# Kernel optimization log

Measured on AMD Instinct MI355X. Metric: run time of the kernel, lower is better.

## Reference

```python
import jax, jax.numpy as jnp
import numpy as np

H = 768
NH = 12
HD = H // NH
NDIM = 5
LN_EPS = 1e-5


def setup_inputs() -> dict:
    key = jax.random.key(0)
    ks = jax.random.split(key, 12)
    B, S = 4, 2048
    xavier = lambda k: jax.random.uniform(k, (H, H), jnp.float32, -1.0, 1.0) * np.sqrt(6.0 / (H + H))
    return {
        "hidden_states": jax.random.normal(ks[0], (B, S, H), jnp.float32),
        "Wq": xavier(ks[1]), "bq": jnp.zeros((H,), jnp.float32),
        "Wk": xavier(ks[2]), "bk": jnp.zeros((H,), jnp.float32),
        "Wv": xavier(ks[3]), "bv": jnp.zeros((H,), jnp.float32),
        "Wo": xavier(ks[4]), "bo": jnp.zeros((H,), jnp.float32),
        # per-dimension, per-head scalar biases (torch init: zeros; use small randn so grads are non-trivial)
        "dim_biases": 0.02 * jax.random.normal(ks[5], (NDIM, NH), jnp.float32),
        "ln_gamma": jnp.ones((H,), jnp.float32),
        "ln_beta": jnp.zeros((H,), jnp.float32),
        "attention_mask": jax.random.randint(ks[6], (4, 2048), 0, 2, jnp.int32),
        "dimension_idx": 2,
    }


def reference(hidden_states, Wq, bq, Wk, bk, Wv, bv, Wo, bo, dim_biases,
              ln_gamma, ln_beta, attention_mask, dimension_idx):
    B, S, _ = hidden_states.shape
    residual = hidden_states
    # torch nn.Linear: x @ W.T + b
    q = (hidden_states @ Wq.T + bq).reshape(B, S, NH, HD).transpose(0, 2, 1, 3)  # [B,NH,S,HD]
    k = (hidden_states @ Wk.T + bk).reshape(B, S, NH, HD).transpose(0, 2, 1, 3)
    v = (hidden_states @ Wv.T + bv).reshape(B, S, NH, HD).transpose(0, 2, 1, 3)

    scores = jnp.einsum("bhqd,bhkd->bhqk", q, k) / np.sqrt(HD)  # [B,NH,S,S]
    if dimension_idx is not None and dimension_idx < NDIM:
        scores = scores + dim_biases[dimension_idx][None, :, None, None]
    # mask over key positions, broadcast over heads and queries
    scores = jnp.where(attention_mask[:, None, None, :] == 0, -jnp.inf, scores)
    attn = jax.nn.softmax(scores, axis=-1)

    ctx = jnp.einsum("bhqk,bhkd->bhqd", attn, v)  # [B,NH,S,HD]
    ctx = ctx.transpose(0, 2, 1, 3).reshape(B, S, H)
    out = ctx @ Wo.T + bo

    y = out + residual
    mu = jnp.mean(y, axis=-1, keepdims=True)
    var = jnp.var(y, axis=-1, keepdims=True)
    y = (y - mu) / jnp.sqrt(var + LN_EPS) * ln_gamma + ln_beta
    return y
```

## Files before the change

kernel.cpp:

```cpp
#include <hip/hip_runtime.h>
#include <hip/hip_bf16.h>

#define HH    768
#define NHEAD 12
#define HDIM  64
#define BB    4
#define SS    2048
#define MM    (BB*SS)
#define NDIMS 5
#define WEL   (HH*HH)
#define LOG2E 1.44269504088896f
#define QSCALE 0.180336881f

typedef unsigned short u16;
typedef __attribute__((ext_vector_type(8))) short short8;
typedef __attribute__((ext_vector_type(4))) float floatx4;

__device__ __forceinline__ float bf2f(u16 u) {
    return __uint_as_float(((unsigned int)u) << 16);
}
__device__ __forceinline__ u16 f2bf(float f) {
    unsigned int x = __float_as_uint(f);
    unsigned int r = (x + 0x7fffu + ((x >> 16) & 1u)) >> 16;
    return (u16)r;
}
__device__ __forceinline__ unsigned int pack_bf16x2(float a, float b) {
    float2 f2 = make_float2(a, b);
    __hip_bfloat162 h2 = __float22bfloat162_rn(f2);
    return *reinterpret_cast<unsigned int*>(&h2);
}

__global__ __launch_bounds__(256) void f32_to_bf16(
    const float* __restrict__ in, u16* __restrict__ out, int n8)
{
    int i = blockIdx.x * 256 + threadIdx.x;
    if (i >= n8) return;
    float4 a = ((const float4*)in)[i*2];
    float4 b = ((const float4*)in)[i*2 + 1];
    ushort4 lo, hi;
    lo.x = f2bf(a.x); lo.y = f2bf(a.y); lo.z = f2bf(a.z); lo.w = f2bf(a.w);
    hi.x = f2bf(b.x); hi.y = f2bf(b.y); hi.z = f2bf(b.z); hi.w = f2bf(b.w);
    ((ushort4*)out)[i*2]     = lo;
    ((ushort4*)out)[i*2 + 1] = hi;
}

__global__ __launch_bounds__(256) void w_cvt4(
    const float* __restrict__ W0, const float* __restrict__ W1,
    const float* __restrict__ W2, const float* __restrict__ W3,
    u16* __restrict__ out)
{
    const float* src = (blockIdx.y == 0) ? W0 : (blockIdx.y == 1) ? W1
                     : (blockIdx.y == 2) ? W2 : W3;
    u16* dst = out + (size_t)blockIdx.y * WEL;
    int i = blockIdx.x * 256 + threadIdx.x;
    float4 a = ((const float4*)src)[i*2];
    float4 b = ((const float4*)src)[i*2 + 1];
    ushort4 lo, hi;
    lo.x = f2bf(a.x); lo.y = f2bf(a.y); lo.z = f2bf(a.z); lo.w = f2bf(a.w);
    hi.x = f2bf(b.x); hi.y = f2bf(b.y); hi.z = f2bf(b.z); hi.w = f2bf(b.w);
    ((ushort4*)dst)[i*2]     = lo;
    ((ushort4*)dst)[i*2 + 1] = hi;
}

__device__ __forceinline__ void gemm_body_bb(
    const u16* __restrict__ Xb, const u16* __restrict__ Wb,
    const float* __restrict__ bias, u16* __restrict__ out,
    int i0, int j0)
{
    __shared__ u16 Xs[128][40];
    __shared__ u16 Wt[64][40];
    const int t = threadIdx.x;
    const int w = t >> 6, lane = t & 63;
    const int c = lane & 15, qd = lane >> 4;
    const int xrow = t >> 1, xoff = (t & 1) * 16;
    const int wn = t >> 2, woff = (t & 3) * 8;

    floatx4 acc[2][4];
    #pragma unroll
    for (int mt = 0; mt < 2; ++mt)
        #pragma unroll
        for (int nt = 0; nt < 4; ++nt) acc[mt][nt] = (floatx4){0.f,0.f,0.f,0.f};

    for (int k0 = 0; k0 < HH; k0 += 32) {
        uint4 xa  = *(const uint4*)(Xb + (size_t)(i0 + xrow)*HH + k0 + xoff);
        uint4 xb2 = *(const uint4*)(Xb + (size_t)(i0 + xrow)*HH + k0 + xoff + 8);
        uint4 wa  = *(const uint4*)(Wb + (size_t)(j0 + wn)*HH + k0 + woff);
        __syncthreads();
        *(uint4*)&Xs[xrow][xoff]     = xa;
        *(uint4*)&Xs[xrow][xoff + 8] = xb2;
        *(uint4*)&Wt[wn][woff]       = wa;
        __syncthreads();

        short8 a0 = *(const short8*)&Xs[w*32 + c][qd*8];
        short8 a1 = *(const short8*)&Xs[w*32 + 16 + c][qd*8];
        #pragma unroll
        for (int nt = 0; nt < 4; ++nt) {
            short8 bfr = *(const short8*)&Wt[nt*16 + c][qd*8];
            acc[0][nt] = __builtin_amdgcn_mfma_f32_16x16x32_bf16(a0, bfr, acc[0][nt], 0, 0, 0);
            acc[1][nt] = __builtin_amdgcn_mfma_f32_16x16x32_bf16(a1, bfr, acc[1][nt], 0, 0, 0);
        }
    }

    float bv[4];
    #pragma unroll
    for (int nt = 0; nt < 4; ++nt) bv[nt] = bias[j0 + nt*16 + c];
    #pragma unroll
    for (int mt = 0; mt < 2; ++mt)
        #pragma unroll
        for (int nt = 0; nt < 4; ++nt)
            #pragma unroll
            for (int r = 0; r < 4; ++r)
                out[(size_t)(i0 + w*32 + mt*16 + qd*4 + r)*HH + j0 + nt*16 + c] =
                    f2bf(acc[mt][nt][r] + bv[nt]);
}

__global__ __launch_bounds__(256) void gemm_mfma_qkv(
    const u16* __restrict__ Xb, const u16* __restrict__ Wb3,
    const float* __restrict__ bq, const float* __restrict__ bk, const float* __restrict__ bv,
    u16* __restrict__ oq, u16* __restrict__ ok, u16* __restrict__ ov)
{
    const int z = blockIdx.z;
    const u16* W = Wb3 + (size_t)z * WEL;
    const float* bias = (z == 0) ? bq : (z == 1) ? bk : bv;
    u16* out = (z == 0) ? oq : (z == 1) ? ok : ov;
    gemm_body_bb(Xb, W, bias, out, blockIdx.y * 128, blockIdx.x * 64);
}

__global__ __launch_bounds__(256) void gemm_mfma_nt_bb(
    const u16* __restrict__ Xb, const u16* __restrict__ Wb,
    const float* __restrict__ bias, u16* __restrict__ out)
{
    gemm_body_bb(Xb, Wb, bias, out, blockIdx.y * 128, blockIdx.x * 64);
}

__global__ __launch_bounds__(256) void gemm_mfma_nt(
    const u16* __restrict__ Xb, const float* __restrict__ W,
    const float* __restrict__ bias, u16* __restrict__ out)
{
    __shared__ u16 Xs[128][40];
    __shared__ u16 Wt[64][40];
    const int t = threadIdx.x;
    const int w = t >> 6, lane = t & 63;
    const int c = lane & 15, qd = lane >> 4;
    const int i0 = blockIdx.y * 128, j0 = blockIdx.x * 64;
    const int xrow = t >> 1, xoff = (t & 1) * 16;
    const int wn = t >> 2, woff = (t & 3) * 8;

    floatx4 acc[2][4];
    #pragma unroll
    for (int mt = 0; mt < 2; ++mt)
        #pragma unroll
        for (int nt = 0; nt < 4; ++nt) acc[mt][nt] = (floatx4){0.f,0.f,0.f,0.f};

    for (int k0 = 0; k0 < HH; k0 += 32) {
        uint4 xa  = *(const uint4*)(Xb + (size_t)(i0 + xrow)*HH + k0 + xoff);
        uint4 xb2 = *(const uint4*)(Xb + (size_t)(i0 + xrow)*HH + k0 + xoff + 8);
        float4 wa = *(const float4*)(W + (size_t)(j0 + wn)*HH + k0 + woff);
        float4 wb = *(const float4*)(W + (size_t)(j0 + wn)*HH + k0 + woff + 4);
        __syncthreads();
        *(uint4*)&Xs[xrow][xoff]     = xa;
        *(uint4*)&Xs[xrow][xoff + 8] = xb2;
        ushort4 w0, w1;
        w0.x = f2bf(wa.x); w0.y = f2bf(wa.y); w0.z = f2bf(wa.z); w0.w = f2bf(wa.w);
        w1.x = f2bf(wb.x); w1.y = f2bf(wb.y); w1.z = f2bf(wb.z); w1.w = f2bf(wb.w);
        *(ushort4*)&Wt[wn][woff]     = w0;
        *(ushort4*)&Wt[wn][woff + 4] = w1;
        __syncthreads();

        short8 a0 = *(const short8*)&Xs[w*32 + c][qd*8];
        short8 a1 = *(const short8*)&Xs[w*32 + 16 + c][qd*8];
        #pragma unroll
        for (int nt = 0; nt < 4; ++nt) {
            short8 bfr = *(const short8*)&Wt[nt*16 + c][qd*8];
            acc[0][nt] = __builtin_amdgcn_mfma_f32_16x16x32_bf16(a0, bfr, acc[0][nt], 0, 0, 0);
            acc[1][nt] = __builtin_amdgcn_mfma_f32_16x16x32_bf16(a1, bfr, acc[1][nt], 0, 0, 0);
        }
    }

    float bv[4];
    #pragma unroll
    for (int nt = 0; nt < 4; ++nt) bv[nt] = bias[j0 + nt*16 + c];
    #pragma unroll
    for (int mt = 0; mt < 2; ++mt)
        #pragma unroll
        for (int nt = 0; nt < 4; ++nt)
            #pragma unroll
            for (int r = 0; r < 4; ++r)
                out[(size_t)(i0 + w*32 + mt*16 + qd*4 + r)*HH + j0 + nt*16 + c] =
                    f2bf(acc[mt][nt][r] + bv[nt]);
}

__global__ __launch_bounds__(256, 3) void attn_mfma(
    const u16* __restrict__ Q, const u16* __restrict__ K, const u16* __restrict__ V,
    const float* __restrict__ dim_biases, const int* __restrict__ mask,
    const int* __restrict__ dim_idx_p, u16* __restrict__ ctx)
{
    __shared__ u16 Ks[64][72];
    __shared__ u16 Vt[64][72];
    __shared__ u16 Pt[4][2][16][72];
    __shared__ float madd[64];

    const int t = threadIdx.x;
    const int w = t >> 6, lane = t & 63;
    const int c = lane & 15, qd = lane >> 4;
    const int b = blockIdx.z, h = blockIdx.y;
    const int q0 = blockIdx.x * 128;

    const int didx = *dim_idx_p;
    const float db2 = ((didx < NDIMS) ? dim_biases[didx*NHEAD + h] : 0.f) * LOG2E;

    short8 ones;
    #pragma unroll
    for (int j = 0; j < 8; ++j) ones[j] = (short)0x3F80;

    short8 qf[2][2];
    #pragma unroll
    for (int g = 0; g < 2; ++g) {
        const u16* qsrc = Q + ((size_t)(b*SS + q0 + w*32 + g*16 + c))*HH + h*HDIM;
        #pragma unroll
        for (int kc = 0; kc < 2; ++kc) {
            ushort4 u0 = *(const ushort4*)(qsrc + kc*32 + qd*8);
            ushort4 u1 = *(const ushort4*)(qsrc + kc*32 + qd*8 + 4);
            const u16 uu[8] = {u0.x,u0.y,u0.z,u0.w,u1.x,u1.y,u1.z,u1.w};
            #pragma unroll
            for (int j = 0; j < 8; ++j)
                qf[g][kc][j] = (short)f2bf(bf2f(uu[j]) * QSCALE);
        }
    }

    floatx4 o[2][4], lacc[2];
    #pragma unroll
    for (int g = 0; g < 2; ++g) {
        lacc[g] = (floatx4){0.f,0.f,0.f,0.f};
        #pragma unroll
        for (int dt = 0; dt < 4; ++dt) o[g][dt] = (floatx4){0.f,0.f,0.f,0.f};
    }

    const int skey = t >> 2, sdp = (t & 3) * 16;
    const int vkey = t & 63, vdp = (t >> 6) * 16;

    for (int kt = 0; kt < SS/64; ++kt) {
        __syncthreads();
        {
            const u16* ksrc = K + ((size_t)(b*SS + kt*64 + skey))*HH + h*HDIM + sdp;
            *(uint4*)&Ks[skey][sdp]     = *(const uint4*)ksrc;
            *(uint4*)&Ks[skey][sdp + 8] = *(const uint4*)(ksrc + 8);
            const u16* vsrc = V + ((size_t)(b*SS + kt*64 + vkey))*HH + h*HDIM + vdp;
            ushort4 v0 = *(const ushort4*)vsrc;
            ushort4 v1 = *(const ushort4*)(vsrc + 4);
            ushort4 v2 = *(const ushort4*)(vsrc + 8);
            ushort4 v3 = *(const ushort4*)(vsrc + 12);
            const u16 vv[16] = {v0.x,v0.y,v0.z,v0.w, v1.x,v1.y,v1.z,v1.w,
                                v2.x,v2.y,v2.z,v2.w, v3.x,v3.y,v3.z,v3.w};
            #pragma unroll
            for (int i = 0; i < 16; ++i) Vt[vdp + i][vkey] = vv[i];
            if (t < 64)
                madd[t] = (mask[(size_t)b*SS + kt*64 + t] != 0) ? db2 : -1e30f;
        }
        __syncthreads();

        floatx4 z[2][4];
        {
            short8 ka[4][2];
            #pragma unroll
            for (int mt = 0; mt < 4; ++mt) {
                ka[mt][0] = *(const short8*)&Ks[mt*16 + c][qd*8];
                ka[mt][1] = *(const short8*)&Ks[mt*16 + c][32 + qd*8];
            }
            #pragma unroll
            for (int g = 0; g < 2; ++g)
                #pragma unroll
                for (int mt = 0; mt < 4; ++mt) {
                    floatx4 zz = __builtin_amdgcn_mfma_f32_16x16x32_bf16(ka[mt][0], qf[g][0], (floatx4){0.f,0.f,0.f,0.f}, 0, 0, 0);
                    z[g][mt] = __builtin_amdgcn_mfma_f32_16x16x32_bf16(ka[mt][1], qf[g][1], zz, 0, 0, 0);
                }
        }

        #pragma unroll
        for (int g = 0; g < 2; ++g) {
            #pragma unroll
            for (int mt = 0; mt < 4; ++mt) {
                unsigned int pk[2];
                #pragma unroll
                for (int half = 0; half < 2; ++half) {
                    float p0 = __builtin_amdgcn_exp2f(z[g][mt][half*2]     + madd[mt*16 + qd*4 + half*2]);
                    float p1 = __builtin_amdgcn_exp2f(z[g][mt][half*2 + 1] + madd[mt*16 + qd*4 + half*2 + 1]);
                    pk[half] = pack_bf16x2(p0, p1);
                }
                *(uint2*)&Pt[w][g][c][mt*16 + qd*4] = make_uint2(pk[0], pk[1]);
            }
        }

        {
            short8 vt[2][4];
            #pragma unroll
            for (int kc = 0; kc < 2; ++kc)
                #pragma unroll
                for (int dt = 0; dt < 4; ++dt)
                    vt[kc][dt] = *(const short8*)&Vt[dt*16 + c][kc*32 + qd*8];
            #pragma unroll
            for (int g = 0; g < 2; ++g)
                #pragma unroll
                for (int kc = 0; kc < 2; ++kc) {
                    short8 ap = *(const short8*)&Pt[w][g][c][kc*32 + qd*8];
                    lacc[g] = __builtin_amdgcn_mfma_f32_16x16x32_bf16(ap, ones, lacc[g], 0, 0, 0);
                    #pragma unroll
                    for (int dt = 0; dt < 4; ++dt)
                        o[g][dt] = __builtin_amdgcn_mfma_f32_16x16x32_bf16(ap, vt[kc][dt], o[g][dt], 0, 0, 0);
                }
        }
    }

    #pragma unroll
    for (int g = 0; g < 2; ++g) {
        #pragma unroll
        for (int r = 0; r < 4; ++r) {
            float lr = lacc[g][r];
            float inv = (lr > 0.f) ? 1.f / lr : 0.f;
            u16* dst = ctx + ((size_t)(b*SS + q0 + w*32 + g*16 + qd*4 + r))*HH + h*HDIM + c;
            #pragma unroll
            for (int dt = 0; dt < 4; ++dt)
                dst[dt*16] = f2bf(o[g][dt][r] * inv);
        }
    }
}

__global__ __launch_bounds__(256) void add_ln_wave(
    const u16* __restrict__ proj, const float* __restrict__ resid,
    const float* __restrict__ gamma, const float* __restrict__ beta,
    float* __restrict__ out)
{
    const int t = threadIdx.x, w = t >> 6, lane = t & 63;
    const int row = blockIdx.x * 4 + w;
    const size_t base = (size_t)row * HH + lane * 12;
    const int gbase = lane * 12;

    float x[12];
    #pragma unroll
    for (int j = 0; j < 3; ++j) {
        ushort4 p = *(const ushort4*)(proj + base + j*4);
        float4  r = *(const float4*)(resid + base + j*4);
        x[j*4+0] = bf2f(p.x) + r.x;
        x[j*4+1] = bf2f(p.y) + r.y;
        x[j*4+2] = bf2f(p.z) + r.z;
        x[j*4+3] = bf2f(p.w) + r.w;
    }
    float s = 0.f, ss = 0.f;
    #pragma unroll
    for (int j = 0; j < 12; ++j) { s += x[j]; ss += x[j]*x[j]; }
    #pragma unroll
    for (int off = 1; off < 64; off <<= 1) {
        s  += __shfl_xor(s, off);
        ss += __shfl_xor(ss, off);
    }
    float mean = s * (1.f/768.f);
    float var  = ss * (1.f/768.f) - mean*mean;
    float rstd = rsqrtf(fmaxf(var, 0.f) + 1e-5f);
    #pragma unroll
    for (int j = 0; j < 3; ++j) {
        float4 g = *(const float4*)(gamma + gbase + j*4);
        float4 bt = *(const float4*)(beta + gbase + j*4);
        float4 y;
        y.x = (x[j*4+0]-mean)*rstd*g.x + bt.x;
        y.y = (x[j*4+1]-mean)*rstd*g.y + bt.y;
        y.z = (x[j*4+2]-mean)*rstd*g.z + bt.z;
        y.w = (x[j*4+3]-mean)*rstd*g.w + bt.w;
        *(float4*)(out + base + j*4) = y;
    }
}

extern "C" void kernel_launch(void* const* d_in, const int* in_sizes, int n_in,
                              void* d_out, int out_size, void* d_ws, size_t ws_size,
                              hipStream_t stream)
{
    (void)in_sizes; (void)n_in; (void)out_size;
    const float* x    = (const float*)d_in[0];
    const float* Wq   = (const float*)d_in[1];
    const float* bq   = (const float*)d_in[2];
    const float* Wk   = (const float*)d_in[3];
    const float* bk   = (const float*)d_in[4];
    const float* Wv   = (const float*)d_in[5];
    const float* bv   = (const float*)d_in[6];
    const float* Wo   = (const float*)d_in[7];
    const float* bo   = (const float*)d_in[8];
    const float* dimb = (const float*)d_in[9];
    const float* gam  = (const float*)d_in[10];
    const float* bet  = (const float*)d_in[11];
    const int* mask   = (const int*)d_in[12];
    const int* didx   = (const int*)d_in[13];

    const size_t N = (size_t)MM * HH;
    if (ws_size < 4 * N * sizeof(u16)) return;
    u16* ws = (u16*)d_ws;
    u16* q    = ws;
    u16* kbuf = ws + N;
    u16* vbuf = ws + 2*N;
    u16* slot3 = ws + 3*N;
    u16* xb   = slot3;
    u16* ctx  = slot3;
    u16* proj = q;

    const bool bigws = ws_size >= (4 * N + 4 * (size_t)WEL) * sizeof(u16);
    u16* wb = ws + 4 * N;

    dim3 gg(HH/64, MM/128);
    f32_to_bf16<<<(int)(N/8/256), 256, 0, stream>>>(x, xb, (int)(N/8));
    if (bigws) {
        w_cvt4<<<dim3(WEL/8/256, 4), 256, 0, stream>>>(Wq, Wk, Wv, Wo, wb);
        gemm_mfma_qkv<<<dim3(HH/64, MM/128, 3), 256, 0, stream>>>(
            xb, wb, bq, bk, bv, q, kbuf, vbuf);
    } else {
        gemm_mfma_nt<<<gg, 256, 0, stream>>>(xb, Wq, bq, q);
        gemm_mfma_nt<<<gg, 256, 0, stream>>>(xb, Wk, bk, kbuf);
        gemm_mfma_nt<<<gg, 256, 0, stream>>>(xb, Wv, bv, vbuf);
    }
    attn_mfma<<<dim3(SS/128, NHEAD, BB), 256, 0, stream>>>(q, kbuf, vbuf, dimb, mask, didx, ctx);
    if (bigws) gemm_mfma_nt_bb<<<gg, 256, 0, stream>>>(ctx, wb + 3*WEL, bo, proj);
    else       gemm_mfma_nt<<<gg, 256, 0, stream>>>(ctx, Wo, bo, proj);
    add_ln_wave<<<MM/4, 256, 0, stream>>>(proj, x, gam, bet, (float*)d_out);
}
```

Baseline: 290.9 us.

## Use 32x32 MFMA with 128x128 GEMM tiles and pack V transpose as bf16 pairs

Replaces the bf16 projection GEMM body with a 128x128 block tile where each wave computes a 64x64 sub-tile using 32x32x16 MFMA instructions. This raises operand reuse per LDS load and halves the number of output-column blocks. Separately, the attention kernel transposes V into LDS as packed 32-bit pairs of adjacent keys instead of scattered 16-bit stores, which cuts LDS store count and bank conflicts. The larger tiles double W staging in LDS and use more accumulator registers, and the QKV grid becomes smaller.

```diff
diff --git a/kernel.cpp b/kernel.cpp
--- a/kernel.cpp
+++ b/kernel.cpp
@@ -15,6 +15,7 @@
 typedef unsigned short u16;
 typedef __attribute__((ext_vector_type(8))) short short8;
 typedef __attribute__((ext_vector_type(4))) float floatx4;
+typedef __attribute__((ext_vector_type(16))) float floatx16;
 
 __device__ __forceinline__ float bf2f(u16 u) {
     return __uint_as_float(((unsigned int)u) << 16);
@@ -62,59 +63,72 @@
     ((ushort4*)dst)[i*2 + 1] = hi;
 }
 
-__device__ __forceinline__ void gemm_body_bb(
+__device__ __forceinline__ void gemm32_body(
     const u16* __restrict__ Xb, const u16* __restrict__ Wb,
     const float* __restrict__ bias, u16* __restrict__ out,
     int i0, int j0)
 {
     __shared__ u16 Xs[128][40];
-    __shared__ u16 Wt[64][40];
+    __shared__ u16 Wt[128][40];
     const int t = threadIdx.x;
     const int w = t >> 6, lane = t & 63;
-    const int c = lane & 15, qd = lane >> 4;
-    const int xrow = t >> 1, xoff = (t & 1) * 16;
-    const int wn = t >> 2, woff = (t & 3) * 8;
-
-    floatx4 acc[2][4];
-    #pragma unroll
-    for (int mt = 0; mt < 2; ++mt)
-        #pragma unroll
-        for (int nt = 0; nt < 4; ++nt) acc[mt][nt] = (floatx4){0.f,0.f,0.f,0.f};
+    const int wy = w >> 1, wx = w & 1;
+    const int m = lane & 31, h = lane >> 5;
+    const int srow = t >> 1, schunk = (t & 1) * 16;
+
+    floatx16 acc[2][2];
+    #pragma unroll
+    for (int am = 0; am < 2; ++am)
+        #pragma unroll
+        for (int bn = 0; bn < 2; ++bn)
+            #pragma unroll
+            for (int r = 0; r < 16; ++r) acc[am][bn][r] = 0.f;
 
     for (int k0 = 0; k0 < HH; k0 += 32) {
-        uint4 xa  = *(const uint4*)(Xb + (size_t)(i0 + xrow)*HH + k0 + xoff);
-        uint4 xb2 = *(const uint4*)(Xb + (size_t)(i0 + xrow)*HH + k0 + xoff + 8);
-        uint4 wa  = *(const uint4*)(Wb + (size_t)(j0 + wn)*HH + k0 + woff);
-        __syncthreads();
-        *(uint4*)&Xs[xrow][xoff]     = xa;
-        *(uint4*)&Xs[xrow][xoff + 8] = xb2;
-        *(uint4*)&Wt[wn][woff]       = wa;
-        __syncthreads();
-
-        short8 a0 = *(const short8*)&Xs[w*32 + c][qd*8];
-        short8 a1 = *(const short8*)&Xs[w*32 + 16 + c][qd*8];
-        #pragma unroll
-        for (int nt = 0; nt < 4; ++nt) {
-            short8 bfr = *(const short8*)&Wt[nt*16 + c][qd*8];
-            acc[0][nt] = __builtin_amdgcn_mfma_f32_16x16x32_bf16(a0, bfr, acc[0][nt], 0, 0, 0);
-            acc[1][nt] = __builtin_amdgcn_mfma_f32_16x16x32_bf16(a1, bfr, acc[1][nt], 0, 0, 0);
-        }
-    }
-
-    float bv[4];
-    #pragma unroll
-    for (int nt = 0; nt < 4; ++nt) bv[nt] = bias[j0 + nt*16 + c];
-    #pragma unroll
-    for (int mt = 0; mt < 2; ++mt)
-        #pragma unroll
-        for (int nt = 0; nt < 4; ++nt)
-            #pragma unroll
-            for (int r = 0; r < 4; ++r)
-                out[(size_t)(i0 + w*32 + mt*16 + qd*4 + r)*HH + j0 + nt*16 + c] =
-                    f2bf(acc[mt][nt][r] + bv[nt]);
-}
-
-__global__ __launch_bounds__(256) void gemm_mfma_qkv(
+        uint4 xa = *(const uint4*)(Xb + (size_t)(i0 + srow)*HH + k0 + schunk);
+        uint4 xc = *(const uint4*)(Xb + (size_t)(i0 + srow)*HH + k0 + schunk + 8);
+        uint4 wa = *(const uint4*)(Wb + (size_t)(j0 + srow)*HH + k0 + schunk);
+        uint4 wc = *(const uint4*)(Wb + (size_t)(j0 + srow)*HH + k0 + schunk + 8);
+        __syncthreads();
+        *(uint4*)&Xs[srow][schunk]     = xa;
+        *(uint4*)&Xs[srow][schunk + 8] = xc;
+        *(uint4*)&Wt[srow][schunk]     = wa;
+        *(uint4*)&Wt[srow][schunk + 8] = wc;
+        __syncthreads();
+
+        #pragma unroll
+        for (int kh = 0; kh < 2; ++kh) {
+            short8 af[2], bf[2];
+            #pragma unroll
+            for (int am = 0; am < 2; ++am)
+                af[am] = *(const short8*)&Xs[wy*64 + am*32 + m][kh*16 + h*8];
+            #pragma unroll
+            for (int bn = 0; bn < 2; ++bn)
+                bf[bn] = *(const short8*)&Wt[wx*64 + bn*32 + m][kh*16 + h*8];
+            #pragma unroll
+            for (int am = 0; am < 2; ++am)
+                #pragma unroll
+                for (int bn = 0; bn < 2; ++bn)
+                    acc[am][bn] = __builtin_amdgcn_mfma_f32_32x32x16_bf16(
+                        af[am], bf[bn], acc[am][bn], 0, 0, 0);
+        }
+    }
+
+    float bb[2];
+    #pragma unroll
+    for (int bn = 0; bn < 2; ++bn) bb[bn] = bias[j0 + wx*64 + bn*32 + m];
+    #pragma unroll
+    for (int am = 0; am < 2; ++am)
+        #pragma unroll
+        for (int bn = 0; bn < 2; ++bn)
+            #pragma unroll
+            for (int r = 0; r < 16; ++r) {
+                int row = i0 + wy*64 + am*32 + (r & 3) + 8*(r >> 2) + 4*h;
+                out[(size_t)row*HH + j0 + wx*64 + bn*32 + m] = f2bf(acc[am][bn][r] + bb[bn]);
+            }
+}
+
+__global__ __launch_bounds__(256) void gemm32_qkv(
     const u16* __restrict__ Xb, const u16* __restrict__ Wb3,
     const float* __restrict__ bq, const float* __restrict__ bk, const float* __restrict__ bv,
     u16* __restrict__ oq, u16* __restrict__ ok, u16* __restrict__ ov)
@@ -123,14 +137,14 @@
     const u16* W = Wb3 + (size_t)z * WEL;
     const float* bias = (z == 0) ? bq : (z == 1) ? bk : bv;
     u16* out = (z == 0) ? oq : (z == 1) ? ok : ov;
-    gemm_body_bb(Xb, W, bias, out, blockIdx.y * 128, blockIdx.x * 64);
-}
-
-__global__ __launch_bounds__(256) void gemm_mfma_nt_bb(
+    gemm32_body(Xb, W, bias, out, blockIdx.y * 128, blockIdx.x * 128);
+}
+
+__global__ __launch_bounds__(256) void gemm32_single(
     const u16* __restrict__ Xb, const u16* __restrict__ Wb,
     const float* __restrict__ bias, u16* __restrict__ out)
 {
-    gemm_body_bb(Xb, Wb, bias, out, blockIdx.y * 128, blockIdx.x * 64);
+    gemm32_body(Xb, Wb, bias, out, blockIdx.y * 128, blockIdx.x * 128);
 }
 
 __global__ __launch_bounds__(256) void gemm_mfma_nt(
@@ -196,7 +210,7 @@
     const int* __restrict__ dim_idx_p, u16* __restrict__ ctx)
 {
     __shared__ u16 Ks[64][72];
-    __shared__ u16 Vt[64][72];
+    __shared__ unsigned int Vt2[64][36];
     __shared__ u16 Pt[4][2][16][72];
     __shared__ float madd[64];
 
@@ -237,7 +251,7 @@
     }
 
     const int skey = t >> 2, sdp = (t & 3) * 16;
-    const int vkey = t & 63, vdp = (t >> 6) * 16;
+    const int vkp = t & 31, vdg = (t >> 5) * 8;
 
     for (int kt = 0; kt < SS/64; ++kt) {
         __syncthreads();
@@ -245,15 +259,17 @@
             const u16* ksrc = K + ((size_t)(b*SS + kt*64 + skey))*HH + h*HDIM + sdp;
             *(uint4*)&Ks[skey][sdp]     = *(const uint4*)ksrc;
             *(uint4*)&Ks[skey][sdp + 8] = *(const uint4*)(ksrc + 8);
-            const u16* vsrc = V + ((size_t)(b*SS + kt*64 + vkey))*HH + h*HDIM + vdp;
-            ushort4 v0 = *(const ushort4*)vsrc;
-            ushort4 v1 = *(const ushort4*)(vsrc + 4);
-            ushort4 v2 = *(const ushort4*)(vsrc + 8);
-            ushort4 v3 = *(const ushort4*)(vsrc + 12);
-            const u16 vv[16] = {v0.x,v0.y,v0.z,v0.w, v1.x,v1.y,v1.z,v1.w,
-                                v2.x,v2.y,v2.z,v2.w, v3.x,v3.y,v3.z,v3.w};
-            #pragma unroll
-            for (int i = 0; i < 16; ++i) Vt[vdp + i][vkey] = vv[i];
+            const u16* va = V + ((size_t)(b*SS + kt*64 + 2*vkp))*HH + h*HDIM + vdg;
+            const u16* vb = va + HH;
+            ushort4 a0 = *(const ushort4*)va;
+            ushort4 a1 = *(const ushort4*)(va + 4);
+            ushort4 b0 = *(const ushort4*)vb;
+            ushort4 b1 = *(const ushort4*)(vb + 4);
+            const u16 aa[8] = {a0.x,a0.y,a0.z,a0.w,a1.x,a1.y,a1.z,a1.w};
+            const u16 bb[8] = {b0.x,b0.y,b0.z,b0.w,b1.x,b1.y,b1.z,b1.w};
+            #pragma unroll
+            for (int i = 0; i < 8; ++i)
+                Vt2[vdg + i][vkp] = (unsigned int)aa[i] | ((unsigned int)bb[i] << 16);
             if (t < 64)
                 madd[t] = (mask[(size_t)b*SS + kt*64 + t] != 0) ? db2 : -1e30f;
         }
@@ -297,7 +313,7 @@
             for (int kc = 0; kc < 2; ++kc)
                 #pragma unroll
                 for (int dt = 0; dt < 4; ++dt)
-                    vt[kc][dt] = *(const short8*)&Vt[dt*16 + c][kc*32 + qd*8];
+                    vt[kc][dt] = *(const short8*)&Vt2[dt*16 + c][kc*16 + qd*4];
             #pragma unroll
             for (int g = 0; g < 2; ++g)
                 #pragma unroll
@@ -403,19 +419,22 @@
     const bool bigws = ws_size >= (4 * N + 4 * (size_t)WEL) * sizeof(u16);
     u16* wb = ws + 4 * N;
 
-    dim3 gg(HH/64, MM/128);
     f32_to_bf16<<<(int)(N/8/256), 256, 0, stream>>>(x, xb, (int)(N/8));
     if (bigws) {
         w_cvt4<<<dim3(WEL/8/256, 4), 256, 0, stream>>>(Wq, Wk, Wv, Wo, wb);
-        gemm_mfma_qkv<<<dim3(HH/64, MM/128, 3), 256, 0, stream>>>(
+        gemm32_qkv<<<dim3(HH/128, MM/128, 3), 256, 0, stream>>>(
             xb, wb, bq, bk, bv, q, kbuf, vbuf);
     } else {
+        dim3 gg(HH/64, MM/128);
         gemm_mfma_nt<<<gg, 256, 0, stream>>>(xb, Wq, bq, q);
         gemm_mfma_nt<<<gg, 256, 0, stream>>>(xb, Wk, bk, kbuf);
         gemm_mfma_nt<<<gg, 256, 0, stream>>>(xb, Wv, bv, vbuf);
     }
     attn_mfma<<<dim3(SS/128, NHEAD, BB), 256, 0, stream>>>(q, kbuf, vbuf, dimb, mask, didx, ctx);
-    if (bigws) gemm_mfma_nt_bb<<<gg, 256, 0, stream>>>(ctx, wb + 3*WEL, bo, proj);
-    else       gemm_mfma_nt<<<gg, 256, 0, stream>>>(ctx, Wo, bo, proj);
+    if (bigws) gemm32_single<<<dim3(HH/128, MM/128), 256, 0, stream>>>(ctx, wb + 3*WEL, bo, proj);
+    else {
+        dim3 gg(HH/64, MM/128);
+        gemm_mfma_nt<<<gg, 256, 0, stream>>>(ctx, Wo, bo, proj);
+    }
     add_ln_wave<<<MM/4, 256, 0, stream>>>(proj, x, gam, bet, (float*)d_out);
 }
```

Measured after the change: 275.7 us. -5.2%, faster.
